# Kernel tuning notes

Hardware: AMD Instinct MI355X
Metric: run time of the kernel (lower is better)

The kernel has to match this reference:

```python
import jax, jax.numpy as jnp
import numpy as np

EPS1 = 1e-8
EPS2 = 1e-5
H_BW = 1.0  # bandwidth h
MSE_W = 1.0
CTX_W = 1.0
PERC_W = 0.02


def _contextual_similarity(out_feat, tgt_feat):
    """Batched contextual similarity (Mechrez et al. 2018).

    out_feat, tgt_feat: [B, C, Hf, Wf]. Returns scalar (mean over batch).
    Matches the torch loop-over-samples / loop-over-target-vectors math,
    fully vectorized as one batched pairwise-cosine + softmax + max.
    """
    B, C = out_feat.shape[0], out_feat.shape[1]
    # X, Y: [B, N, C] with N = Hf*Wf spatial positions
    X = out_feat.reshape(B, C, -1).transpose(0, 2, 1)
    Y = tgt_feat.reshape(B, C, -1).transpose(0, 2, 1)
    X = X - X.mean(axis=1, keepdims=True)  # center per channel over positions
    Y = Y - Y.mean(axis=1, keepdims=True)
    xn = jnp.linalg.norm(X, axis=2)  # [B, N]
    yn = jnp.linalg.norm(Y, axis=2)  # [B, N]
    # cosine distance d[b, x, y] = 1 - <X_x, Y_y> / (|X_x||Y_y| + eps1)
    S = jnp.einsum('bxc,byc->bxy', X, Y)
    d = 1.0 - S / (xn[:, :, None] * yn[:, None, :] + EPS1)
    # normalize by min over target vectors y (torch: dxy.min(dim=0) with dxy [Ny, Nx])
    d_ = d / (d.min(axis=2, keepdims=True) + EPS2)
    w = jnp.exp((1.0 - d_) / H_BW)
    c = w / w.sum(axis=2, keepdims=True)  # softmax over y per x
    # torch: cxy.max(dim=1)[0].mean() -> max over x for each y, mean over y
    CS = c.max(axis=1).mean(axis=1)  # [B]
    return CS.mean()


def _mse(a, b):
    return jnp.mean((a - b) ** 2)


def setup_inputs() -> dict:
    key = jax.random.key(0)
    k1, k2, k3, k4 = jax.random.split(key, 4)
    outputs = jax.random.normal(k1, (4, 3, 256, 256), dtype=jnp.float32)
    targets = jax.random.normal(k2, (4, 3, 256, 256), dtype=jnp.float32)
    output_features = jax.random.normal(k3, (4, 256, 64, 64), dtype=jnp.float32)
    target_features = jax.random.normal(k4, (4, 256, 64, 64), dtype=jnp.float32)
    return {"outputs": outputs, "targets": targets,
            "output_features": output_features, "target_features": target_features}


def reference(outputs, targets, output_features, target_features):
    loss = MSE_W * _mse(outputs, targets)
    loss = loss - CTX_W * jnp.log(_contextual_similarity(output_features, target_features))
    loss = loss + PERC_W * _mse(output_features, target_features)
    return loss
```

## Files before the change

### kernel.cpp

```cpp
#include <hip/hip_runtime.h>
#include <hip/hip_bf16.h>
#include <cstdint>

#define EPS2f 1e-5f

typedef __bf16 bf16x8 __attribute__((ext_vector_type(8)));
typedef float floatx4 __attribute__((ext_vector_type(4)));
typedef _Float16 half8 __attribute__((ext_vector_type(8)));
typedef __fp16 fp16x2 __attribute__((ext_vector_type(2)));

static constexpr int Bn = 4, Cn = 256, Nn = 4096;

static constexpr size_t MSE1P = 0;
static constexpr size_t MSE2P = 256;
static constexpr size_t CSP   = 1536;
static constexpr size_t MEANX = 2560;
static constexpr size_t MEANY = 3584;
static constexpr size_t IXN   = 4608;
static constexpr size_t IYN   = 20992;
static constexpr size_t DMIN  = 37376;
static constexpr size_t RSUM  = 53760;
static constexpr size_t XCO   = 70144;
static constexpr size_t YCO   = 70144 + 2097152;
static constexpr size_t SOFF  = 70144 + 2 * 2097152;

__device__ __forceinline__ unsigned short f2bf(float f) {
    unsigned u = __float_as_uint(f);
    u += 0x7fffu + ((u >> 16) & 1u);
    return (unsigned short)(u >> 16);
}

__device__ __forceinline__ void stage16(const unsigned short* g, unsigned short* l) {
    __builtin_amdgcn_global_load_lds(
        (const __attribute__((address_space(1))) unsigned int*)g,
        (__attribute__((address_space(3))) unsigned int*)l, 16, 0, 0);
}

__global__ __launch_bounds__(256) void prep1(const float4* __restrict__ outs,
                                             const float4* __restrict__ tgts,
                                             const float4* __restrict__ of4,
                                             const float4* __restrict__ tf4,
                                             float* __restrict__ ws) {
    const int bid = blockIdx.x, t = threadIdx.x;
    __shared__ float red[12];
    if (bid < 1024) {
        const int c = bid & 255, b = bid >> 8;
        const float4* po = of4 + ((size_t)b * Cn + c) * (Nn / 4);
        const float4* pt = tf4 + ((size_t)b * Cn + c) * (Nn / 4);
        float so = 0.f, st = 0.f, sq = 0.f;
        for (int i = t; i < 1024; i += 256) {
            float4 o = po[i], q = pt[i];
            so += o.x + o.y + o.z + o.w;
            st += q.x + q.y + q.z + q.w;
            float dx = o.x - q.x, dy = o.y - q.y, dz = o.z - q.z, dw = o.w - q.w;
            sq += dx * dx + dy * dy + dz * dz + dw * dw;
        }
        for (int m = 1; m < 64; m <<= 1) {
            so += __shfl_xor(so, m); st += __shfl_xor(st, m); sq += __shfl_xor(sq, m);
        }
        if ((t & 63) == 0) { int w = t >> 6; red[w * 3] = so; red[w * 3 + 1] = st; red[w * 3 + 2] = sq; }
        __syncthreads();
        if (t == 0) {
            so = red[0] + red[3] + red[6] + red[9];
            st = red[1] + red[4] + red[7] + red[10];
            sq = red[2] + red[5] + red[8] + red[11];
            ws[MEANX + b * Cn + c] = so * (1.f / 4096.f);
            ws[MEANY + b * Cn + c] = st * (1.f / 4096.f);
            ws[MSE2P + bid] = sq;
        }
    } else if (bid < 1216) {
        const int base = bid - 1024;
        float sq = 0.f;
        for (int i = base * 256 + t; i < 196608; i += 192 * 256) {
            float4 a = outs[i], b4 = tgts[i];
            float dx = a.x - b4.x, dy = a.y - b4.y, dz = a.z - b4.z, dw = a.w - b4.w;
            sq += dx * dx + dy * dy + dz * dz + dw * dw;
        }
        for (int m = 1; m < 64; m <<= 1) sq += __shfl_xor(sq, m);
        if ((t & 63) == 0) red[t >> 6] = sq;
        __syncthreads();
        if (t == 0) ws[MSE1P + base] = red[0] + red[1] + red[2] + red[3];
    } else {
        const int i = (bid - 1216) * 256 + t;
        ws[DMIN + i] = (i < 16384) ? __builtin_inff() : 0.f;
    }
}

__global__ __launch_bounds__(256) void center_fused(const float* __restrict__ ofeat,
                                                    const float* __restrict__ tfeat,
                                                    float* __restrict__ ws) {
    const int b = blockIdx.y, nb = blockIdx.x, z = blockIdx.z;
    const float* feat = z ? tfeat : ofeat;
    const float* mean = ws + (z ? MEANY : MEANX);
    unsigned short* outb = (unsigned short*)(ws + (z ? YCO : XCO));
    float* inv = ws + (z ? IYN : IXN);
    __shared__ float mean_s[256];
    __shared__ float sq_s[256];
    const int t = threadIdx.x;
    mean_s[t] = mean[b * Cn + t];
    __syncthreads();
    const int pos = t & 63, cg = t >> 6;
    const int n = nb * 64 + pos;
    const float* fb = feat + (size_t)b * Cn * Nn;
    unsigned short* ob = outb + ((size_t)b * Nn + n) * Cn;
    float ss = 0.f;
    for (int c0 = cg * 64; c0 < cg * 64 + 64; c0 += 8) {
        unsigned short tmp[8];
        #pragma unroll
        for (int u = 0; u < 8; ++u) {
            float v = fb[(size_t)(c0 + u) * Nn + n] - mean_s[c0 + u];
            ss += v * v;
            tmp[u] = f2bf(v);
        }
        uint4 pk;
        pk.x = (unsigned)tmp[0] | ((unsigned)tmp[1] << 16);
        pk.y = (unsigned)tmp[2] | ((unsigned)tmp[3] << 16);
        pk.z = (unsigned)tmp[4] | ((unsigned)tmp[5] << 16);
        pk.w = (unsigned)tmp[6] | ((unsigned)tmp[7] << 16);
        *(uint4*)(ob + c0) = pk;
    }
    sq_s[t] = ss;
    __syncthreads();
    if (t < 64) {
        float s = sq_s[t] + sq_s[t + 64] + sq_s[t + 128] + sq_s[t + 192];
        inv[(size_t)b * Nn + nb * 64 + t] = 1.f / sqrtf(s);
    }
}

__global__ __launch_bounds__(256) void gemm_store(const unsigned short* __restrict__ Xc,
                                                  const unsigned short* __restrict__ Yc,
                                                  const float* __restrict__ ixn,
                                                  const float* __restrict__ iyn,
                                                  float* __restrict__ dmin,
                                                  _Float16* __restrict__ S) {
    __shared__ __align__(16) unsigned short smem[16384];
    __shared__ float ixn_s[128], iyn_s[128];

    const int t = threadIdx.x;
    const int lin = blockIdx.x;
    const int xcd = lin & 7, idx = lin >> 3;
    const int b = xcd >> 1;
    const int by = (xcd & 1) * 16 + (idx & 15);
    const int bx = idx >> 4;
    const size_t nb = (size_t)b * Nn;

    if (t < 128) ixn_s[t] = ixn[nb + bx * 128 + t];
    else iyn_s[t - 128] = iyn[nb + by * 128 + (t - 128)];

    const int wid = t >> 6, lane = t & 63;
    const int wm = wid >> 1, wn = wid & 1;
    const int lr = lane & 15, lq = lane >> 4;

    const unsigned short* Ag = Xc + (nb + bx * 128) * Cn;
    const unsigned short* Bg =Yc + (nb + by * 128) * Cn;
    const int lrow = lane >> 2, lsl = (lane & 3) * 8;
    const unsigned short* gA = Ag + (size_t)(wid * 32 + lrow) * Cn + lsl;
    const unsigned short* gB = Bg + (size_t)(wid * 32 + lrow) * Cn + lsl;
    const int w1024 = wid * 1024;

    floatx4 acc[4][4];
    #pragma unroll
    for (int i = 0; i < 4; i++)
        #pragma unroll
        for (int j = 0; j < 4; j++) acc[i][j] = (floatx4){0.f, 0.f, 0.f, 0.f};

    stage16(gA, smem + w1024);
    stage16(gA + 16 * Cn, smem + w1024 + 512);
    stage16(gB, smem + 4096 + w1024);
    stage16(gB + 16 * Cn, smem + 4096 + w1024 + 512);
    __syncthreads();

    #pragma unroll
    for (int ks = 0; ks < 8; ks++) {
        const int cur = (ks & 1) * 8192, nxt = 8192 - cur;
        if (ks < 7) {
            const int koff = (ks + 1) * 32;
            stage16(gA + koff, smem + nxt + w1024);
            stage16(gA + koff + 16 * Cn, smem + nxt + w1024 + 512);
            stage16(gB + koff, smem + nxt + 4096 + w1024);
            stage16(gB + koff + 16 * Cn, smem + nxt + 4096 + w1024 + 512);
        }
        bf16x8 af[4], bv[4];
        #pragma unroll
        for (int i = 0; i < 4; i++)
            af[i] = *(const bf16x8*)(smem + cur + (wm * 64 + i * 16 + lr) * 32 + lq * 8);
        #pragma unroll
        for (int j = 0; j < 4; j++)
            bv[j] = *(const bf16x8*)(smem + cur + 4096 + (wn * 64 + j * 16 + lr) * 32 + lq * 8);
        #pragma unroll
        for (int i = 0; i < 4; i++)
            #pragma unroll
            for (int j = 0; j < 4; j++)
                acc[i][j] = __builtin_amdgcn_mfma_f32_16x16x32_bf16(af[i], bv[j], acc[i][j], 0, 0, 0);
        if (ks < 7) __syncthreads();
    }

    float ix[16];
    #pragma unroll
    for (int i = 0; i < 4; i++)
        #pragma unroll
        for (int r = 0; r < 4; r++) ix[i * 4 + r] = ixn_s[wm * 64 + i * 16 + lq * 4 + r];
    float rmin[16];
    #pragma unroll
    for (int k = 0; k < 16; k++) rmin[k] = __builtin_inff();
    #pragma unroll
    for (int i = 0; i < 4; i++)
        #pragma unroll
        for (int j = 0; j < 4; j++) {
            const float iy = iyn_s[wn * 64 + j * 16 + lr];
            #pragma unroll
            for (int r = 0; r < 4; r++)
                rmin[i * 4 + r] = fminf(rmin[i * 4 + r], 1.f - acc[i][j][r] * ix[i * 4 + r] * iy);
        }
    #pragma unroll
    for (int m = 1; m < 16; m <<= 1)
        #pragma unroll
        for (int k = 0; k < 16; k++) rmin[k] = fminf(rmin[k], __shfl_xor(rmin[k], m));
    if (lr == 0) {
        #pragma unroll
        for (int i = 0; i < 4; i++)
            #pragma unroll
            for (int r = 0; r < 4; r++)
                atomicMin((int*)&dmin[nb + bx * 128 + wm * 64 + i * 16 + lq * 4 + r],
                          __float_as_int(rmin[i * 4 + r]));
    }
    __syncthreads();

    #pragma unroll
    for (int i = 0; i < 4; i++) {
        const int xlocal = wm * 64 + i * 16 + lq * 4;
        #pragma unroll
        for (int j = 0; j < 4; j++) {
            const int ylocal = wn * 64 + j * 16 + lr;
            const float iy = iyn_s[ylocal];
            float c0 = acc[i][j][0] * ix[i * 4 + 0] * iy;
            float c1 = acc[i][j][1] * ix[i * 4 + 1] * iy;
            float c2 = acc[i][j][2] * ix[i * 4 + 2] * iy;
            float c3 = acc[i][j][3] * ix[i * 4 + 3] * iy;
            fp16x2 p0 = __builtin_amdgcn_cvt_pkrtz(c0, c1);
            fp16x2 p1 = __builtin_amdgcn_cvt_pkrtz(c2, c3);
            *(float2*)(smem + ylocal * 128 + (xlocal ^ ((ylocal & 15) * 8))) =
                make_float2(__builtin_bit_cast(float, p0), __builtin_bit_cast(float, p1));
        }
    }
    __syncthreads();

    #pragma unroll
    for (int p = 0; p < 8; p++) {
        const int yl = wid * 32 + p * 4 + (lane >> 4);
        const int ch = lane & 15;
        uint4 v = *(const uint4*)(smem + yl * 128 + ((ch * 8) ^ ((yl & 15) * 8)));
        *(uint4*)(S + (nb + by * 128 + yl) * (size_t)Nn + bx * 128 + ch * 8) = v;
    }
}

__global__ __launch_bounds__(256) void b1_rsum(const _Float16* __restrict__ S,
                                               const float* __restrict__ dmin,
                                               float* __restrict__ rsum) {
    __shared__ float red[32 * 65];
    const int t = threadIdx.x;
    const int x0 = blockIdx.x * 64, ys = blockIdx.y, b = blockIdx.z;
    const int chunk = t & 7, yg = t >> 3;
    const int xbase = x0 + chunk * 8;
    const size_t gb = (size_t)b * Nn;

    float invd[8], av[8];
    #pragma unroll
    for (int u = 0; u < 8; u++) {
        float dm = dmin[gb + xbase + u];
        invd[u] = 1.f / (dm + EPS2f);
        av[u] = 1.f - invd[u];
    }
    float s[8];
    #pragma unroll
    for (int u = 0; u < 8; u++) s[u] = 0.f;

    for (int k = 0; k < 16; k++) {
        const int y = ys * 512 + yg + 32 * k;
        half8 hv = *(const half8*)(S + (gb + y) * Nn + xbase);
        #pragma unroll
        for (int u = 0; u < 8; u++)
            s[u] += __expf(fmaf((float)hv[u], invd[u], av[u]));
    }
    #pragma unroll
    for (int u = 0; u < 8; u++) red[yg * 65 + chunk * 8 + u] = s[u];
    __syncthreads();
    if (t < 64) {
        float rs = 0.f;
        #pragma unroll 8
        for (int g = 0; g < 32; g++) rs += red[g * 65 + t];
        atomicAdd(&rsum[gb + x0 + t], rs);
    }
}

__global__ __launch_bounds__(256) void b2_cmax(const _Float16* __restrict__ S,
                                               const float* __restrict__ dmin,
                                               const float* __restrict__ rsum,
                                               float* __restrict__ csp) {
    __shared__ float ps[512 * 20];
    __shared__ float red2[16];
    const int t = threadIdx.x, b = blockIdx.y;
    const size_t gb = (size_t)b * Nn;
    for (int i = t; i < Nn; i += 256) {
        float iv = 1.f / (dmin[gb + i] + EPS2f);
        float gg = 1.f - iv - __logf(rsum[gb + i]);
        int c = i >> 3, e = i & 7;
        ps[c * 20 + e * 2] = iv;
        ps[c * 20 + e * 2 + 1] = gg;
    }
    __syncthreads();

    const int lanegrp = t & 15, yloc = t >> 4;
    const int y = blockIdx.x * 16 + yloc;
    const _Float16* Sy = S + (gb + y) * Nn;

    float cm = 0.f;
    for (int k = 0; k < 32; k++) {
        const int chunk = lanegrp + 16 * k;
        half8 hv = *(const half8*)(Sy + chunk * 8);
        const float* pp = &ps[chunk * 20];
        float4 p01 = *(const float4*)(pp);
        float4 p23 = *(const float4*)(pp + 4);
        float4 p45 = *(const float4*)(pp + 8);
        float4 p67 = *(const float4*)(pp + 12);
        float iv[8] = {p01.x, p01.z, p23.x, p23.z, p45.x, p45.z, p67.x, p67.z};
        float gg[8] = {p01.y, p01.w, p23.y, p23.w, p45.y, p45.w, p67.y, p67.w};
        #pragma unroll
        for (int u = 0; u < 8; u++)
            cm = fmaxf(cm, __expf(fmaf((float)hv[u], iv[u], gg[u])));
    }
    #pragma unroll
    for (int m = 1; m < 16; m <<= 1) cm = fmaxf(cm, __shfl_xor(cm, m));
    if (lanegrp == 0) red2[yloc] = cm;
    __syncthreads();
    if (t == 0) {
        float s2 = 0.f;
        #pragma unroll
        for (int i = 0; i < 16; i++) s2 += red2[i];
        csp[b * 256 + blockIdx.x] = s2;
    }
}

__global__ __launch_bounds__(256) void finalize_kernel(const float* __restrict__ ws,
                                                       float* __restrict__ out) {
    const int t = threadIdx.x;
    float s1 = 0.f, s2 = 0.f, s3 = 0.f;
    if (t < 192) s1 = ws[MSE1P + t];
    for (int i = t; i < 1024; i += 256) { s2 += ws[MSE2P + i]; s3 += ws[CSP + i]; }
    for (int m = 1; m < 64; m <<= 1) {
        s1 += __shfl_xor(s1, m); s2 += __shfl_xor(s2, m); s3 += __shfl_xor(s3, m);
    }
    __shared__ float red[12];
    if ((t & 63) == 0) { int w = t >> 6; red[w * 3] = s1; red[w * 3 + 1] = s2; red[w * 3 + 2] = s3; }
    __syncthreads();
    if (t == 0) {
        s1 = red[0] + red[3] + red[6] + red[9];
        s2 = red[1] + red[4] + red[7] + red[10];
        s3 = red[2] + red[5] + red[8] + red[11];
        float cs = s3 * (1.f / 16384.f);
        out[0] = s1 * (1.f / 786432.f) - logf(cs) + 0.02f * s2 * (1.f / 4194304.f);
    }
}

extern "C" void kernel_launch(void* const* d_in, const int* in_sizes, int n_in,
                              void* d_out, int out_size, void* d_ws, size_t ws_size,
                              hipStream_t stream) {
    const float* outputs = (const float*)d_in[0];
    const float* targets = (const float*)d_in[1];
    const float* ofeat   = (const float*)d_in[2];
    const float* tfeat   = (const float*)d_in[3];
    float* ws  = (float*)d_ws;
    float* out = (float*)d_out;

    unsigned short* Xc = (unsigned short*)(ws + XCO);
    unsigned short* Yc = (unsigned short*)(ws + YCO);
    _Float16* S = (_Float16*)(ws + SOFF);

    prep1<<<1344, 256, 0, stream>>>((const float4*)outputs, (const float4*)targets,
                                    (const float4*)ofeat, (const float4*)tfeat, ws);
    center_fused<<<dim3(Nn / 64, Bn, 2), 256, 0, stream>>>(ofeat, tfeat, ws);
    gemm_store<<<4096, 256, 0, stream>>>(Xc, Yc, ws + IXN, ws + IYN, ws + DMIN, S);
    b1_rsum<<<dim3(64, 8, Bn), 256, 0, stream>>>(S, ws + DMIN, ws + RSUM);
    b2_cmax<<<dim3(Nn / 16, Bn), 256, 0, stream>>>(S, ws + DMIN, ws + RSUM, ws + CSP);
    finalize_kernel<<<1, 256, 0, stream>>>(ws, out);
}
```

Before: 257.2 us.

## Rework GEMM staging to register prefetch and use exp2 with hoisted max-exp

The GEMM kernel drops direct global-to-LDS loads and instead prefetches the next K-slice (now 64 wide, double-buffered in a larger LDS tile with a k-major layout) into registers while MFMAs run on the current slice. The norm scales are read straight from global into registers, which removes the shared arrays and one barrier. The softmax kernels fold log2(e) into the coefficients and use exp2f. The column-max kernel takes the max of the exponent argument and applies a single exp2 after the reduction, so it no longer computes one exponential per element. The larger LDS footprint and the register prefetch buffers may lower occupancy.

```diff
diff --git a/kernel.cpp b/kernel.cpp
--- a/kernel.cpp
+++ b/kernel.cpp
@@ -3,6 +3,7 @@
 #include <cstdint>
 
 #define EPS2f 1e-5f
+#define LOG2E 1.44269504f
 
 typedef __bf16 bf16x8 __attribute__((ext_vector_type(8)));
 typedef float floatx4 __attribute__((ext_vector_type(4)));
@@ -28,12 +29,6 @@
     unsigned u = __float_as_uint(f);
     u += 0x7fffu + ((u >> 16) & 1u);
     return (unsigned short)(u >> 16);
-}
-
-__device__ __forceinline__ void stage16(const unsigned short* g, unsigned short* l) {
-    __builtin_amdgcn_global_load_lds(
-        (const __attribute__((address_space(1))) unsigned int*)g,
-        (__attribute__((address_space(3))) unsigned int*)l, 16, 0, 0);
 }
 
 __global__ __launch_bounds__(256) void prep1(const float4* __restrict__ outs,
@@ -133,8 +128,7 @@
                                                   const float* __restrict__ iyn,
                                                   float* __restrict__ dmin,
                                                   _Float16* __restrict__ S) {
-    __shared__ __align__(16) unsigned short smem[16384];
-    __shared__ float ixn_s[128], iyn_s[128];
+    __shared__ __align__(16) unsigned short smem[32768];
 
     const int t = threadIdx.x;
     const int lin = blockIdx.x;
@@ -144,19 +138,16 @@
     const int bx = idx >> 4;
     const size_t nb = (size_t)b * Nn;
 
-    if (t < 128) ixn_s[t] = ixn[nb + bx * 128 + t];
-    else iyn_s[t - 128] = iyn[nb + by * 128 + (t - 128)];
-
     const int wid = t >> 6, lane = t & 63;
     const int wm = wid >> 1, wn = wid & 1;
     const int lr = lane & 15, lq = lane >> 4;
 
+    const int srow = t >> 3, sq8 = t & 7;
     const unsigned short* Ag = Xc + (nb + bx * 128) * Cn;
-    const unsigned short* Bg =Yc + (nb + by * 128) * Cn;
-    const int lrow = lane >> 2, lsl = (lane & 3) * 8;
-    const unsigned short* gA = Ag + (size_t)(wid * 32 + lrow) * Cn + lsl;
-    const unsigned short* gB = Bg + (size_t)(wid * 32 + lrow) * Cn + lsl;
-    const int w1024 = wid * 1024;
+    const unsigned short* Bg = Yc + (nb + by * 128) * Cn;
+    const unsigned short* gA = Ag + (size_t)srow * Cn + sq8 * 8;
+    const unsigned short* gB = Bg + (size_t)srow * Cn + sq8 * 8;
+    const int wofs = (sq8 * 128 + srow) * 8;
 
     floatx4 acc[4][4];
     #pragma unroll
@@ -164,42 +155,69 @@
         #pragma unroll
         for (int j = 0; j < 4; j++) acc[i][j] = (floatx4){0.f, 0.f, 0.f, 0.f};
 
-    stage16(gA, smem + w1024);
-    stage16(gA + 16 * Cn, smem + w1024 + 512);
-    stage16(gB, smem + 4096 + w1024);
-    stage16(gB + 16 * Cn, smem + 4096 + w1024 + 512);
-    __syncthreads();
-
-    #pragma unroll
-    for (int ks = 0; ks < 8; ks++) {
-        const int cur = (ks & 1) * 8192, nxt = 8192 - cur;
-        if (ks < 7) {
-            const int koff = (ks + 1) * 32;
-            stage16(gA + koff, smem + nxt + w1024);
-            stage16(gA + koff + 16 * Cn, smem + nxt + w1024 + 512);
-            stage16(gB + koff, smem + nxt + 4096 + w1024);
-            stage16(gB + koff + 16 * Cn, smem + nxt + 4096 + w1024 + 512);
-        }
-        bf16x8 af[4], bv[4];
-        #pragma unroll
-        for (int i = 0; i < 4; i++)
-            af[i] = *(const bf16x8*)(smem + cur + (wm * 64 + i * 16 + lr) * 32 + lq * 8);
-        #pragma unroll
-        for (int j = 0; j < 4; j++)
-            bv[j] = *(const bf16x8*)(smem + cur + 4096 + (wn * 64 + j * 16 + lr) * 32 + lq * 8);
-        #pragma unroll
-        for (int i = 0; i < 4; i++)
+    {
+        uint4 pa[4], pb[4];
+        #pragma unroll
+        for (int g = 0; g < 4; g++) {
+            pa[g] = *(const uint4*)(gA + (size_t)g * 32 * Cn);
+            pb[g] = *(const uint4*)(gB + (size_t)g * 32 * Cn);
+        }
+        #pragma unroll
+        for (int g = 0; g < 4; g++) {
+            *(uint4*)(smem + wofs + g * 256) = pa[g];
+            *(uint4*)(smem + 8192 + wofs + g * 256) = pb[g];
+        }
+    }
+    __syncthreads();
+
+    #pragma unroll
+    for (int ks = 0; ks < 4; ks++) {
+        const int cur = (ks & 1) * 16384, nxt = 16384 - cur;
+        uint4 pa[4], pb[4];
+        if (ks < 3) {
+            const int koff = (ks + 1) * 64;
+            #pragma unroll
+            for (int g = 0; g < 4; g++) {
+                pa[g] = *(const uint4*)(gA + (size_t)g * 32 * Cn + koff);
+                pb[g] = *(const uint4*)(gB + (size_t)g * 32 * Cn + koff);
+            }
+        }
+        #pragma unroll
+        for (int sc = 0; sc < 2; sc++) {
+            const int kq = (sc * 4 + lq) * 1024;
+            bf16x8 af[4], bv[4];
+            #pragma unroll
+            for (int i = 0; i < 4; i++)
+                af[i] = *(const bf16x8*)(smem + cur + kq + (wm * 64 + i * 16 + lr) * 8);
             #pragma unroll
             for (int j = 0; j < 4; j++)
-                acc[i][j] = __builtin_amdgcn_mfma_f32_16x16x32_bf16(af[i], bv[j], acc[i][j], 0, 0, 0);
-        if (ks < 7) __syncthreads();
-    }
-
-    float ix[16];
+                bv[j] = *(const bf16x8*)(smem + cur + 8192 + kq + (wn * 64 + j * 16 + lr) * 8);
+            #pragma unroll
+            for (int i = 0; i < 4; i++)
+                #pragma unroll
+                for (int j = 0; j < 4; j++)
+                    acc[i][j] = __builtin_amdgcn_mfma_f32_16x16x32_bf16(af[i], bv[j], acc[i][j], 0, 0, 0);
+        }
+        if (ks < 3) {
+            #pragma unroll
+            for (int g = 0; g < 4; g++) {
+                *(uint4*)(smem + nxt + wofs + g * 256) = pa[g];
+                *(uint4*)(smem + nxt + 8192 + wofs + g * 256) = pb[g];
+            }
+            __syncthreads();
+        }
+    }
+
+    float ix[16], iyv[4];
     #pragma unroll
     for (int i = 0; i < 4; i++)
         #pragma unroll
-        for (int r = 0; r < 4; r++) ix[i * 4 + r] = ixn_s[wm * 64 + i * 16 + lq * 4 + r];
+        for (int r = 0; r < 4; r++)
+            ix[i * 4 + r] = ixn[nb + bx * 128 + wm * 64 + i * 16 + lq * 4 + r];
+    #pragma unroll
+    for (int j = 0; j < 4; j++)
+        iyv[j] = iyn[nb + by * 128 + wn * 64 + j * 16 + lr];
+
     float rmin[16];
     #pragma unroll
     for (int k = 0; k < 16; k++) rmin[k] = __builtin_inff();
@@ -207,10 +225,9 @@
     for (int i = 0; i < 4; i++)
         #pragma unroll
         for (int j = 0; j < 4; j++) {
-            const float iy = iyn_s[wn * 64 + j * 16 + lr];
             #pragma unroll
             for (int r = 0; r < 4; r++)
-                rmin[i * 4 + r] = fminf(rmin[i * 4 + r], 1.f - acc[i][j][r] * ix[i * 4 + r] * iy);
+                rmin[i * 4 + r] = fminf(rmin[i * 4 + r], 1.f - acc[i][j][r] * ix[i * 4 + r] * iyv[j]);
         }
     #pragma unroll
     for (int m = 1; m < 16; m <<= 1)
@@ -224,7 +241,6 @@
                 atomicMin((int*)&dmin[nb + bx * 128 + wm * 64 + i * 16 + lq * 4 + r],
                           __float_as_int(rmin[i * 4 + r]));
     }
-    __syncthreads();
 
     #pragma unroll
     for (int i = 0; i < 4; i++) {
@@ -232,7 +248,7 @@
         #pragma unroll
         for (int j = 0; j < 4; j++) {
             const int ylocal = wn * 64 + j * 16 + lr;
-            const float iy = iyn_s[ylocal];
+            const float iy = iyv[j];
             float c0 = acc[i][j][0] * ix[i * 4 + 0] * iy;
             float c1 = acc[i][j][1] * ix[i * 4 + 1] * iy;
             float c2 = acc[i][j][2] * ix[i * 4 + 2] * iy;
@@ -264,12 +280,12 @@
     const int xbase = x0 + chunk * 8;
     const size_t gb = (size_t)b * Nn;
 
-    float invd[8], av[8];
+    float ivl[8], avl[8];
     #pragma unroll
     for (int u = 0; u < 8; u++) {
-        float dm = dmin[gb + xbase + u];
-        invd[u] = 1.f / (dm + EPS2f);
-        av[u] = 1.f - invd[u];
+        float iv = 1.f / (dmin[gb + xbase + u] + EPS2f);
+        ivl[u] = iv * LOG2E;
+        avl[u] = (1.f - iv) * LOG2E;
     }
     float s[8];
     #pragma unroll
@@ -280,7 +296,7 @@
         half8 hv = *(const half8*)(S + (gb + y) * Nn + xbase);
         #pragma unroll
         for (int u = 0; u < 8; u++)
-            s[u] += __expf(fmaf((float)hv[u], invd[u], av[u]));
+            s[u] += exp2f(fmaf((float)hv[u], ivl[u], avl[u]));
     }
     #pragma unroll
     for (int u = 0; u < 8; u++) red[yg * 65 + chunk * 8 + u] = s[u];
@@ -303,10 +319,11 @@
     const size_t gb = (size_t)b * Nn;
     for (int i = t; i < Nn; i += 256) {
         float iv = 1.f / (dmin[gb + i] + EPS2f);
-        float gg = 1.f - iv - __logf(rsum[gb + i]);
+        float ivl = iv * LOG2E;
+        float ggl = (1.f - iv) * LOG2E - __log2f(rsum[gb + i]);
         int c = i >> 3, e = i & 7;
-        ps[c * 20 + e * 2] = iv;
-        ps[c * 20 + e * 2 + 1] = gg;
+        ps[c * 20 + e * 2] = ivl;
+        ps[c * 20 + e * 2 + 1] = ggl;
     }
     __syncthreads();
 
@@ -314,7 +331,7 @@
     const int y = blockIdx.x * 16 + yloc;
     const _Float16* Sy = S + (gb + y) * Nn;
 
-    float cm = 0.f;
+    float cm = -1e30f;
     for (int k = 0; k < 32; k++) {
         const int chunk = lanegrp + 16 * k;
         half8 hv = *(const half8*)(Sy + chunk * 8);
@@ -327,11 +344,11 @@
         float gg[8] = {p01.y, p01.w, p23.y, p23.w, p45.y, p45.w, p67.y, p67.w};
         #pragma unroll
         for (int u = 0; u < 8; u++)
-            cm = fmaxf(cm, __expf(fmaf((float)hv[u], iv[u], gg[u])));
+            cm = fmaxf(cm, fmaf((float)hv[u], iv[u], gg[u]));
     }
     #pragma unroll
     for (int m = 1; m < 16; m <<= 1) cm = fmaxf(cm, __shfl_xor(cm, m));
-    if (lanegrp == 0) red2[yloc] = cm;
+    if (lanegrp == 0) red2[yloc] = exp2f(cm);
     __syncthreads();
     if (t == 0) {
         float s2 = 0.f;
```

Result: slower. 280.0 us (+8.9%).
